# Kernel tuning notes

Hardware: AMD Instinct MI355X
Metric: run time of the kernel (lower is better)

Reference implementation:

```python
import jax, jax.numpy as jnp
import numpy as np

S, D, H, E, A = 30, 200, 200, 1024, 6
B, T = 1024, 64


def setup_inputs() -> dict:
    key = jax.random.key(0)
    ks = jax.random.split(key, 32)
    rn = lambda k, sh, sc=0.05: jax.random.normal(k, sh, dtype=jnp.float32) * sc
    inp = {
        'embed': rn(ks[0], (B, T, E), 1.0),
        'action': rn(ks[1], (B, T, A), 1.0),
        'noise_prior': rn(ks[2], (T, B, S), 1.0),
        'noise_post': rn(ks[3], (T, B, S), 1.0),
        # img1: Dense(hidden) on [stoch+action]
        'w_img1': rn(ks[4], (S + A, H)), 'b_img1': jnp.zeros((H,), jnp.float32),
        # GRUCell(deter): kernel [in,3*D] (z,r,h order), recurrent kernel, 2 biases (reset_after=True)
        'gru_w': rn(ks[5], (H, 3 * D)), 'gru_u': rn(ks[6], (D, 3 * D)),
        'gru_b': jnp.zeros((3 * D,), jnp.float32), 'gru_rb': jnp.zeros((3 * D,), jnp.float32),
        'w_img2': rn(ks[7], (D, H)), 'b_img2': jnp.zeros((H,), jnp.float32),
        'w_imean': rn(ks[8], (H, S)), 'b_imean': jnp.zeros((S,), jnp.float32),
        'w_istd': rn(ks[9], (H, S)), 'b_istd': jnp.zeros((S,), jnp.float32),
        # obs1: Dense(hidden) on [deter+embed]
        'w_obs1': rn(ks[10], (D + E, H)), 'b_obs1': jnp.zeros((H,), jnp.float32),
        'w_omean': rn(ks[11], (H, S)), 'b_omean': jnp.zeros((S,), jnp.float32),
        'w_ostd': rn(ks[12], (H, S)), 'b_ostd': jnp.zeros((S,), jnp.float32),
    }
    return inp


def _observe(embed, action, noise_prior, noise_post,
             w_img1, b_img1, gru_w, gru_u, gru_b, gru_rb,
             w_img2, b_img2, w_imean, b_imean, w_istd, b_istd,
             w_obs1, b_obs1, w_omean, b_omean, w_ostd, b_ostd):
    elu = jax.nn.elu
    Bsz = action.shape[0]

    def step(carry, xs):
        stoch, deter = carry  # [B,S], [B,D]
        a, e, nz_p, nz_o = xs
        # ---- img_step (prior) ----
        x = elu(jnp.concatenate([stoch, a], -1) @ w_img1 + b_img1)  # [B,H]
        xg = x @ gru_w + gru_b          # [B,3D]
        hg = deter @ gru_u + gru_rb     # [B,3D] (reset_after)
        xz, xr, xh = jnp.split(xg, 3, -1)
        hz, hr, hh = jnp.split(hg, 3, -1)
        z = jax.nn.sigmoid(xz + hz)
        r = jax.nn.sigmoid(xr + hr)
        hhat = jnp.tanh(xh + r * hh)
        deter_n = z * deter + (1.0 - z) * hhat  # [B,D]
        x2 = elu(deter_n @ w_img2 + b_img2)
        pmean = x2 @ w_imean + b_imean
        pstd = jax.nn.softplus(x2 @ w_istd + b_istd) + 0.1
        pstoch = pmean + pstd * nz_p
        # ---- obs_step (posterior) ----
        xo = elu(jnp.concatenate([deter_n, e], -1) @ w_obs1 + b_obs1)
        omean = xo @ w_omean + b_omean
        ostd = jax.nn.softplus(xo @ w_ostd + b_ostd)
        ostoch = omean + ostd * nz_o
        out = jnp.concatenate([omean, ostd, ostoch, deter_n,
                               pmean, pstd, pstoch, deter_n], -1)  # [B, 580]
        return (ostoch, deter_n), out

    init = (jnp.zeros((Bsz, S), embed.dtype), jnp.zeros((Bsz, D), embed.dtype))
    xs = (jnp.transpose(action, (1, 0, 2)), jnp.transpose(embed, (1, 0, 2)),
          noise_prior, noise_post)
    _, ys = jax.lax.scan(step, init, xs)  # [T,B,580]
    return jnp.transpose(ys, (1, 0, 2))   # [B,T,580] = post(mean,std,stoch,deter) ++ prior(...)


def reference(embed, action, noise_prior, noise_post,
              w_img1, b_img1, gru_w, gru_u, gru_b, gru_rb,
              w_img2, b_img2, w_imean, b_imean, w_istd, b_istd,
              w_obs1, b_obs1, w_omean, b_omean, w_ostd, b_ostd):
    return _observe(embed, action, noise_prior, noise_post,
                    w_img1, b_img1, gru_w, gru_u, gru_b, gru_rb,
                    w_img2, b_img2, w_imean, b_imean, w_istd, b_istd,
                    w_obs1, b_obs1, w_omean, b_omean, w_ostd, b_ostd)
```

## Files before the change

### kernel.cpp

```cpp
#include <hip/hip_runtime.h>
#include <cstddef>


typedef __bf16 bf16x8 __attribute__((ext_vector_type(8)));
typedef float  f32x4  __attribute__((ext_vector_type(4)));

#define OFF_K1WT 0
#define OFF_W1F  212992
#define OFF_GWF  226304
#define OFF_GUF  362496
#define OFF_WCF  498688
#define OFF_WHF  591872
#define WS_BF_TOTAL 620544
#define WS_XPRE_BYTES 1241088

__device__ __forceinline__ float elu1(float v){ return v > 0.f ? v : expm1f(v); }
__device__ __forceinline__ float sigm(float v){ return 1.f / (1.f + expf(-v)); }
__device__ __forceinline__ float spls(float v){ return fmaxf(v,0.f) + log1pf(expf(-fabsf(v))); }

__global__ __launch_bounds__(256) void k0_convert(
    const float* __restrict__ w_img1, const float* __restrict__ gru_w,
    const float* __restrict__ gru_u,  const float* __restrict__ w_img2,
    const float* __restrict__ w_imean, const float* __restrict__ w_istd,
    const float* __restrict__ w_obs1, const float* __restrict__ w_omean,
    const float* __restrict__ w_ostd, __bf16* __restrict__ o)
{
  int i = blockIdx.x * 256 + threadIdx.x;
  if (i >= WS_BF_TOTAL) return;
  float v = 0.f;
  if (i < OFF_W1F) {
    int n = i >> 10, k = i & 1023;
    v = (n < 200) ? w_obs1[(size_t)(200 + k) * 200 + n] : 0.f;
  } else if (i < OFF_GWF) {
    int q = i - OFF_W1F;
    int e = q & 7, lane = (q >> 3) & 63, f = q >> 9;
    int kc = f & 1, tt = f >> 1;
    int n  = tt * 16 + (lane & 15);
    int kk = kc * 32 + (lane >> 4) * 8 + e;
    if (n < 200 && kk < 36) v = w_img1[kk * 200 + n];
  } else if (i < OFF_GUF) {
    int q = i - OFF_GWF;
    int e = q & 7, lane = (q >> 3) & 63, f = q >> 9;
    int k = f % 7, tt = f / 7;
    int j  = tt * 16 + (lane & 15);
    int kk = k * 32 + (lane >> 4) * 8 + e;
    if (j < 600 && kk < 200) v = gru_w[kk * 600 + j];
  } else if (i < OFF_WCF) {
    int q = i - OFF_GUF;
    int e = q & 7, lane = (q >> 3) & 63, f = q >> 9;
    int k = f % 7, tt = f / 7;
    int j  = tt * 16 + (lane & 15);
    int kk = k * 32 + (lane >> 4) * 8 + e;
    if (j < 600 && kk < 200) v = gru_u[kk * 600 + j];
  } else if (i < OFF_WHF) {
    int q = i - OFF_WCF;
    int e = q & 7, lane = (q >> 3) & 63, f = q >> 9;
    int k = f % 7, tt = f / 7;
    int kk = k * 32 + (lane >> 4) * 8 + e;
    if (kk < 200) {
      if (tt < 13) {
        int n = tt * 16 + (lane & 15);
        if (n < 200) v = w_img2[kk * 200 + n];
      } else {
        int n = (tt - 13) * 16 + (lane & 15);
        if (n < 200) v = w_obs1[kk * 200 + n];
      }
    }
  } else {
    int q = i - OFF_WHF;
    int e = q & 7, lane = (q >> 3) & 63, f = q >> 9;
    int k = f % 7, tt = f / 7;
    int kk = k * 32 + (lane >> 4) * 8 + e;
    int n = tt * 16 + (lane & 15);
    int h = n >> 5, c = n & 31;
    if (kk < 200 && c < 30) {
      const float* wh = (h == 0) ? w_omean : (h == 1) ? w_ostd : (h == 2) ? w_imean : w_istd;
      v = wh[kk * 30 + c];
    }
  }
  o[i] = (__bf16)v;
}

__global__ __launch_bounds__(256) void k1_embed_gemm(
    const float* __restrict__ embed, const __bf16* __restrict__ wT,
    const float* __restrict__ b_obs1, float* __restrict__ xpre)
{
  __shared__ __align__(16) __bf16 As[64][72];
  __shared__ __align__(16) __bf16 Bs[208][72];
  int tid = threadIdx.x;
  int b = blockIdx.x;
  int wave = tid >> 6, lane = tid & 63;
  int lm = lane & 15, quad = lane >> 4;

  f32x4 acc[13];
#pragma unroll
  for (int n = 0; n < 13; ++n) acc[n] = (f32x4){0.f, 0.f, 0.f, 0.f};

  const float* arow_base = embed + (size_t)b * 64 * 1024;

  for (int ko = 0; ko < 1024; ko += 64) {
#pragma unroll
    for (int p = 0; p < 4; ++p) {
      int v = p * 256 + tid; int row = v >> 4; int c4 = v & 15;
      float4 f = *(const float4*)(arow_base + (size_t)row * 1024 + ko + c4 * 4);
      __bf16* dst = &As[row][c4 * 4];
      dst[0] = (__bf16)f.x; dst[1] = (__bf16)f.y;
      dst[2] = (__bf16)f.z; dst[3] = (__bf16)f.w;
    }
#pragma unroll
    for (int p = 0; p < 13; ++p) {
      int v = p * 256 + tid; int n = v >> 4; int c4 = v & 15;
      ushort4 u = *(const ushort4*)(wT + (size_t)n * 1024 + ko + c4 * 4);
      *(ushort4*)&Bs[n][c4 * 4] = u;
    }
    __syncthreads();
#pragma unroll
    for (int kc = 0; kc < 2; ++kc) {
      bf16x8 a = *(const bf16x8*)&As[16 * wave + lm][kc * 32 + quad * 8];
#pragma unroll
      for (int n = 0; n < 13; ++n) {
        bf16x8 bb = *(const bf16x8*)&Bs[16 * n + lm][kc * 32 + quad * 8];
        acc[n] = __builtin_amdgcn_mfma_f32_16x16x32_bf16(a, bb, acc[n], 0, 0, 0);
      }
    }
    __syncthreads();
  }
  int trow_base = 16 * wave + quad * 4;
#pragma unroll
  for (int n = 0; n < 13; ++n) {
    int col = n * 16 + lm;
    if (col < 200) {
      float bias = b_obs1[col];
#pragma unroll
      for (int r = 0; r < 4; ++r) {
        int trow = trow_base + r;
        xpre[(size_t)trow * (1024 * 200) + (size_t)b * 200 + col] = acc[n][r] + bias;
      }
    }
  }
}

__global__ __launch_bounds__(512) void k2_recurrent(
    const float* __restrict__ action, const float* __restrict__ noise_prior,
    const float* __restrict__ noise_post,
    const float* __restrict__ b_img1, const float* __restrict__ gru_b,
    const float* __restrict__ gru_rb, const float* __restrict__ b_img2,
    const float* __restrict__ b_imean, const float* __restrict__ b_istd,
    const float* __restrict__ b_omean, const float* __restrict__ b_ostd,
    const __bf16* __restrict__ w1F, const __bf16* __restrict__ gwF,
    const __bf16* __restrict__ guF, const __bf16* __restrict__ wcF,
    const __bf16* __restrict__ whF,
    const float* __restrict__ xpre, float* __restrict__ out)
{
  __shared__ __align__(16) __bf16 actin[16][72];
  __shared__ __align__(16) __bf16 xbuf[16][232];
  __shared__ __align__(16) __bf16 dbuf[16][232];
  __shared__ __align__(16) char   ovl[39168];
  __shared__ float biasL[1760];

  const int tid  = threadIdx.x;
  const int wv   = tid >> 6;
  const int lane = tid & 63;
  const int lm   = lane & 15, quad = lane >> 4;
  const int b0   = blockIdx.x * 16;

  __bf16* gg    = (__bf16*)ovl;
  __bf16* x2b   = (__bf16*)ovl;
  __bf16* xob   = (__bf16*)(ovl + 7424);
  float*  headb = (float*)(ovl + 14848);

  for (int i = tid; i < 16 * 72; i += 512) {
    int m = i / 72, c = i - m * 72;
    if (c < 30 || c >= 36) actin[m][c] = (__bf16)0.f;
  }
  for (int i = tid; i < 16 * 232; i += 512) { ((__bf16*)xbuf)[i] = (__bf16)0.f; ((__bf16*)dbuf)[i] = (__bf16)0.f; }
  for (int i = tid; i < 1760; i += 512) {
    float v = 0.f;
    if (i < 208)       { if (i < 200) v = b_img1[i]; }
    else if (i < 816)  { int j = i - 208;  if (j < 600) v = gru_b[j]; }
    else if (i < 1424) { int j = i - 816;  if (j < 600) v = gru_rb[j]; }
    else if (i < 1632) { int j = i - 1424; if (j < 200) v = b_img2[j]; }
    else { int n = i - 1632; int h = n >> 5, c = n & 31;
           if (c < 30) v = ((h == 0) ? b_omean : (h == 1) ? b_ostd : (h == 2) ? b_imean : b_istd)[c]; }
    biasL[i] = v;
  }
  if (tid < 96) {
    int m = tid / 6, k = tid - m * 6;
    actin[m][30 + k] = (__bf16)action[(size_t)(b0 + m) * 384 + k];
  }
  __syncthreads();

  for (int t = 0; t < 64; ++t) {
    for (int tt = wv; tt < 13; tt += 8) {
      const __bf16* bw = w1F + tt * 1024 + lane * 8;
      bf16x8 a0 = *(const bf16x8*)&actin[lm][quad * 8];
      bf16x8 a1 = *(const bf16x8*)&actin[lm][32 + quad * 8];
      bf16x8 bv0 = *(const bf16x8*)(bw);
      bf16x8 bv1 = *(const bf16x8*)(bw + 512);
      f32x4 c = (f32x4){0.f, 0.f, 0.f, 0.f};
      c = __builtin_amdgcn_mfma_f32_16x16x32_bf16(a0, bv0, c, 0, 0, 0);
      c = __builtin_amdgcn_mfma_f32_16x16x32_bf16(a1, bv1, c, 0, 0, 0);
      int col = tt * 16 + lm;
      float bias = biasL[col];
      if (col < 200) {
#pragma unroll
        for (int r = 0; r < 4; ++r) xbuf[quad * 4 + r][col] = (__bf16)elu1(c[r] + bias);
      }
    }
    __syncthreads();

    {
      const int gsel = wv >> 2, wsub = wv & 3;
      const __bf16* WF    = gsel ? guF : gwF;
      const __bf16* Abase = gsel ? &dbuf[0][0] : &xbuf[0][0];
      const int cbase = gsel ? 608 : 0;
      const int bbase = gsel ? 816 : 208;
      bf16x8 af[7];
#pragma unroll
      for (int k = 0; k < 7; ++k) af[k] = *(const bf16x8*)(Abase + lm * 232 + k * 32 + quad * 8);
      for (int tt = wsub; tt < 38; tt += 4) {
        const __bf16* bw = WF + tt * 3584 + lane * 8;
        f32x4 c = (f32x4){0.f, 0.f, 0.f, 0.f};
#pragma unroll
        for (int k = 0; k < 7; ++k) {
          bf16x8 bv = *(const bf16x8*)(bw + k * 512);
          c = __builtin_amdgcn_mfma_f32_16x16x32_bf16(af[k], bv, c, 0, 0, 0);
        }
        int col = tt * 16 + lm;
        float bias = biasL[bbase + col];
#pragma unroll
        for (int r = 0; r < 4; ++r) gg[(quad * 4 + r) * 1224 + cbase + col] = (__bf16)(c[r] + bias);
      }
    }
    __syncthreads();

    for (int idx = tid; idx < 3200; idx += 512) {
      int m = idx / 200, d = idx - m * 200;
      const __bf16* row = gg + m * 1224;
      float xz = (float)row[d],        xr_ = (float)row[200 + d], xh = (float)row[400 + d];
      float hz = (float)row[608 + d],  hr_ = (float)row[808 + d], hh = (float)row[1008 + d];
      float z  = sigm(xz + hz);
      float rr = sigm(xr_ + hr_);
      float hc = tanhf(xh + rr * hh);
      float dn = z * (float)dbuf[m][d] + (1.f - z) * hc;
      dbuf[m][d] = (__bf16)dn;
      size_t ob = ((size_t)(b0 + m) * 64 + t) * 580;
      out[ob + 90 + d]  = dn;
      out[ob + 380 + d] = dn;
    }
    __syncthreads();

    {
      bf16x8 df[7];
#pragma unroll
      for (int k = 0; k < 7; ++k) df[k] = *(const bf16x8*)(&dbuf[lm][0] + k * 32 + quad * 8);
      for (int tt = wv; tt < 26; tt += 8) {
        const __bf16* bw = wcF + tt * 3584 + lane * 8;
        f32x4 c = (f32x4){0.f, 0.f, 0.f, 0.f};
#pragma unroll
        for (int k = 0; k < 7; ++k) {
          bf16x8 bv = *(const bf16x8*)(bw + k * 512);
          c = __builtin_amdgcn_mfma_f32_16x16x32_bf16(df[k], bv, c, 0, 0, 0);
        }
        if (tt < 13) {
          int col = tt * 16 + lm;
          float bias = biasL[1424 + col];
          if (col < 200) {
#pragma unroll
            for (int r = 0; r < 4; ++r) x2b[(quad * 4 + r) * 232 + col] = (__bf16)elu1(c[r] + bias);
          }
        } else {
          int col = (tt - 13) * 16 + lm;
          if (col < 200) {
#pragma unroll
            for (int r = 0; r < 4; ++r) {
              int m2 = quad * 4 + r;
              float pre = c[r] + xpre[((size_t)t * 1024 + b0 + m2) * 200 + col];
              xob[m2 * 232 + col] = (__bf16)elu1(pre);
            }
          }
        }
      }
    }
    __syncthreads();

    {
      const __bf16* Ab = (wv < 4) ? xob : x2b;
      bf16x8 hf[7];
#pragma unroll
      for (int k = 0; k < 7; ++k) hf[k] = *(const bf16x8*)(Ab + lm * 232 + k * 32 + quad * 8);
      const __bf16* bw = whF + wv * 3584 + lane * 8;
      f32x4 c = (f32x4){0.f, 0.f, 0.f, 0.f};
#pragma unroll
      for (int k = 0; k < 7; ++k) {
        bf16x8 bv = *(const bf16x8*)(bw + k * 512);
        c = __builtin_amdgcn_mfma_f32_16x16x32_bf16(hf[k], bv, c, 0, 0, 0);
      }
      int n = wv * 16 + lm;
      float bias = biasL[1632 + n];
#pragma unroll
      for (int r = 0; r < 4; ++r) headb[(quad * 4 + r) * 132 + n] = c[r] + bias;
    }
    __syncthreads();

    if (tid < 480) {
      int m = tid / 30, c = tid - m * 30;
      const float* hb = headb + m * 132;
      float om = hb[c], osr = hb[32 + c], pm = hb[64 + c], psr = hb[96 + c];
      float os = spls(osr);
      float ps = spls(psr) + 0.1f;
      float nzo = noise_post [(size_t)t * 30720 + (b0 + m) * 30 + c];
      float nzp = noise_prior[(size_t)t * 30720 + (b0 + m) * 30 + c];
      float ost = om + os * nzo;
      float pst = pm + ps * nzp;
      actin[m][c] = (__bf16)ost;
      size_t ob = ((size_t)(b0 + m) * 64 + t) * 580;
      out[ob + c]       = om;
      out[ob + 30 + c]  = os;
      out[ob + 60 + c]  = ost;
      out[ob + 290 + c] = pm;
      out[ob + 320 + c] = ps;
      out[ob + 350 + c] = pst;
    } else if (t < 63) {
      for (int j = tid - 480; j < 96; j += 32) {
        int m = j / 6, k = j - m * 6;
        actin[m][30 + k] = (__bf16)action[(size_t)(b0 + m) * 384 + (t + 1) * 6 + k];
      }
    }
    __syncthreads();
  }
}

extern "C" void kernel_launch(void* const* d_in, const int* in_sizes, int n_in,
                              void* d_out, int out_size, void* d_ws, size_t ws_size,
                              hipStream_t stream) {
  const float* embed   = (const float*)d_in[0];
  const float* action  = (const float*)d_in[1];
  const float* nzp     = (const float*)d_in[2];
  const float* nzo     = (const float*)d_in[3];
  const float* w_img1  = (const float*)d_in[4];
  const float* b_img1  = (const float*)d_in[5];
  const float* gru_w   = (const float*)d_in[6];
  const float* gru_u   = (const float*)d_in[7];
  const float* gru_b   = (const float*)d_in[8];
  const float* gru_rb  = (const float*)d_in[9];
  const float* w_img2  = (const float*)d_in[10];
  const float* b_img2  = (const float*)d_in[11];
  const float* w_imean = (const float*)d_in[12];
  const float* b_imean = (const float*)d_in[13];
  const float* w_istd  = (const float*)d_in[14];
  const float* b_istd  = (const float*)d_in[15];
  const float* w_obs1  = (const float*)d_in[16];
  const float* b_obs1  = (const float*)d_in[17];
  const float* w_omean = (const float*)d_in[18];
  const float* b_omean = (const float*)d_in[19];
  const float* w_ostd  = (const float*)d_in[20];
  const float* b_ostd  = (const float*)d_in[21];
  float* out = (float*)d_out;

  __bf16* wbf = (__bf16*)d_ws;
  float* xpre = (float*)((char*)d_ws + WS_XPRE_BYTES);

  k0_convert<<<(WS_BF_TOTAL + 255) / 256, 256, 0, stream>>>(
      w_img1, gru_w, gru_u, w_img2, w_imean, w_istd, w_obs1, w_omean, w_ostd, wbf);

  k1_embed_gemm<<<1024, 256, 0, stream>>>(embed, wbf + OFF_K1WT, b_obs1, xpre);

  k2_recurrent<<<64, 512, 0, stream>>>(
      action, nzp, nzo,
      b_img1, gru_b, gru_rb, b_img2, b_imean, b_istd, b_omean, b_ostd,
      wbf + OFF_W1F, wbf + OFF_GWF, wbf + OFF_GUF, wbf + OFF_WCF, wbf + OFF_WHF,
      xpre, out);
}
```

Before: 1.675 ms.

## Double recurrent block to 1024 threads and prefetch weights, noise and xpre

Raises the recurrent kernel block size from 512 to 1024 threads so each per-step GEMM phase is split across 16 waves instead of 8. Idle waves in the first phase stage the noise tiles into shared memory and preload the obs1 precomputed activations before they are needed. The GRU GEMM loop double-buffers weight fragments from global memory. The MFMA chains are split into two accumulators for more instruction-level parallelism, and tanh is replaced with a sigmoid-based formula. The larger block raises register pressure (at most 64 VGPRs per thread at 1024 threads), which may cause spills given the prefetch buffers.

```diff
diff --git a/kernel.cpp b/kernel.cpp
--- a/kernel.cpp
+++ b/kernel.cpp
@@ -140,7 +140,7 @@
   }
 }
 
-__global__ __launch_bounds__(512) void k2_recurrent(
+__global__ __launch_bounds__(1024) void k2_recurrent(
     const float* __restrict__ action, const float* __restrict__ noise_prior,
     const float* __restrict__ noise_post,
     const float* __restrict__ b_img1, const float* __restrict__ gru_b,
@@ -157,6 +157,7 @@
   __shared__ __align__(16) __bf16 dbuf[16][232];
   __shared__ __align__(16) char   ovl[39168];
   __shared__ float biasL[1760];
+  __shared__ float noiseb[960];
 
   const int tid  = threadIdx.x;
   const int wv   = tid >> 6;
@@ -169,12 +170,12 @@
   __bf16* xob   = (__bf16*)(ovl + 7424);
   float*  headb = (float*)(ovl + 14848);
 
-  for (int i = tid; i < 16 * 72; i += 512) {
+  for (int i = tid; i < 16 * 72; i += 1024) {
     int m = i / 72, c = i - m * 72;
     if (c < 30 || c >= 36) actin[m][c] = (__bf16)0.f;
   }
-  for (int i = tid; i < 16 * 232; i += 512) { ((__bf16*)xbuf)[i] = (__bf16)0.f; ((__bf16*)dbuf)[i] = (__bf16)0.f; }
-  for (int i = tid; i < 1760; i += 512) {
+  for (int i = tid; i < 16 * 232; i += 1024) { ((__bf16*)xbuf)[i] = (__bf16)0.f; ((__bf16*)dbuf)[i] = (__bf16)0.f; }
+  for (int i = tid; i < 1760; i += 1024) {
     float v = 0.f;
     if (i < 208)       { if (i < 200) v = b_img1[i]; }
     else if (i < 816)  { int j = i - 208;  if (j < 600) v = gru_b[j]; }
@@ -191,8 +192,8 @@
   __syncthreads();
 
   for (int t = 0; t < 64; ++t) {
-    for (int tt = wv; tt < 13; tt += 8) {
-      const __bf16* bw = w1F + tt * 1024 + lane * 8;
+    if (wv < 13) {
+      const __bf16* bw = w1F + wv * 1024 + lane * 8;
       bf16x8 a0 = *(const bf16x8*)&actin[lm][quad * 8];
       bf16x8 a1 = *(const bf16x8*)&actin[lm][32 + quad * 8];
       bf16x8 bv0 = *(const bf16x8*)(bw);
@@ -200,17 +201,38 @@
       f32x4 c = (f32x4){0.f, 0.f, 0.f, 0.f};
       c = __builtin_amdgcn_mfma_f32_16x16x32_bf16(a0, bv0, c, 0, 0, 0);
       c = __builtin_amdgcn_mfma_f32_16x16x32_bf16(a1, bv1, c, 0, 0, 0);
-      int col = tt * 16 + lm;
+      int col = wv * 16 + lm;
       float bias = biasL[col];
       if (col < 200) {
 #pragma unroll
         for (int r = 0; r < 4; ++r) xbuf[quad * 4 + r][col] = (__bf16)elu1(c[r] + bias);
       }
-    }
-    __syncthreads();
-
+    } else {
+      int j = (wv - 13) * 64 + lane;
+      const float* np = noise_post  + (size_t)t * 30720 + (size_t)b0 * 30;
+      const float* nq = noise_prior + (size_t)t * 30720 + (size_t)b0 * 30;
+      for (int q = j; q < 480; q += 192) {
+        noiseb[q]       = np[q];
+        noiseb[480 + q] = nq[q];
+      }
+    }
+    __syncthreads();
+
+    float xp[4] = {0.f, 0.f, 0.f, 0.f};
     {
-      const int gsel = wv >> 2, wsub = wv & 3;
+      int tt_xo = (wv >= 13) ? wv : (wv < 10 ? wv + 16 : -1);
+      if (tt_xo >= 0) {
+        int col0 = (tt_xo - 13) * 16 + lm;
+        if (col0 < 200) {
+#pragma unroll
+          for (int r = 0; r < 4; ++r)
+            xp[r] = xpre[((size_t)t * 1024 + b0 + quad * 4 + r) * 200 + col0];
+        }
+      }
+    }
+
+    {
+      const int gsel = wv >> 3, wsub = wv & 7;
       const __bf16* WF    = gsel ? guF : gwF;
       const __bf16* Abase = gsel ? &dbuf[0][0] : &xbuf[0][0];
       const int cbase = gsel ? 608 : 0;
@@ -218,30 +240,47 @@
       bf16x8 af[7];
 #pragma unroll
       for (int k = 0; k < 7; ++k) af[k] = *(const bf16x8*)(Abase + lm * 232 + k * 32 + quad * 8);
-      for (int tt = wsub; tt < 38; tt += 4) {
-        const __bf16* bw = WF + tt * 3584 + lane * 8;
-        f32x4 c = (f32x4){0.f, 0.f, 0.f, 0.f};
-#pragma unroll
-        for (int k = 0; k < 7; ++k) {
-          bf16x8 bv = *(const bf16x8*)(bw + k * 512);
-          c = __builtin_amdgcn_mfma_f32_16x16x32_bf16(af[k], bv, c, 0, 0, 0);
+      bf16x8 cur[7], nxt[7];
+      {
+        const __bf16* bw = WF + (size_t)wsub * 3584 + lane * 8;
+#pragma unroll
+        for (int k = 0; k < 7; ++k) cur[k] = *(const bf16x8*)(bw + k * 512);
+      }
+      for (int tt = wsub; tt < 38; tt += 8) {
+        int tn = tt + 8;
+        if (tn < 38) {
+          const __bf16* bn = WF + (size_t)tn * 3584 + lane * 8;
+#pragma unroll
+          for (int k = 0; k < 7; ++k) nxt[k] = *(const bf16x8*)(bn + k * 512);
         }
+        f32x4 c0 = (f32x4){0.f, 0.f, 0.f, 0.f};
+        f32x4 c1 = (f32x4){0.f, 0.f, 0.f, 0.f};
+        c0 = __builtin_amdgcn_mfma_f32_16x16x32_bf16(af[0], cur[0], c0, 0, 0, 0);
+        c1 = __builtin_amdgcn_mfma_f32_16x16x32_bf16(af[1], cur[1], c1, 0, 0, 0);
+        c0 = __builtin_amdgcn_mfma_f32_16x16x32_bf16(af[2], cur[2], c0, 0, 0, 0);
+        c1 = __builtin_amdgcn_mfma_f32_16x16x32_bf16(af[3], cur[3], c1, 0, 0, 0);
+        c0 = __builtin_amdgcn_mfma_f32_16x16x32_bf16(af[4], cur[4], c0, 0, 0, 0);
+        c1 = __builtin_amdgcn_mfma_f32_16x16x32_bf16(af[5], cur[5], c1, 0, 0, 0);
+        c0 = __builtin_amdgcn_mfma_f32_16x16x32_bf16(af[6], cur[6], c0, 0, 0, 0);
+        f32x4 c = c0 + c1;
         int col = tt * 16 + lm;
         float bias = biasL[bbase + col];
 #pragma unroll
         for (int r = 0; r < 4; ++r) gg[(quad * 4 + r) * 1224 + cbase + col] = (__bf16)(c[r] + bias);
-      }
-    }
-    __syncthreads();
-
-    for (int idx = tid; idx < 3200; idx += 512) {
+#pragma unroll
+        for (int k = 0; k < 7; ++k) cur[k] = nxt[k];
+      }
+    }
+    __syncthreads();
+
+    for (int idx = tid; idx < 3200; idx += 1024) {
       int m = idx / 200, d = idx - m * 200;
       const __bf16* row = gg + m * 1224;
       float xz = (float)row[d],        xr_ = (float)row[200 + d], xh = (float)row[400 + d];
       float hz = (float)row[608 + d],  hr_ = (float)row[808 + d], hh = (float)row[1008 + d];
       float z  = sigm(xz + hz);
       float rr = sigm(xr_ + hr_);
-      float hc = tanhf(xh + rr * hh);
+      float hc = 2.f * sigm(2.f * (xh + rr * hh)) - 1.f;
       float dn = z * (float)dbuf[m][d] + (1.f - z) * hc;
       dbuf[m][d] = (__bf16)dn;
       size_t ob = ((size_t)(b0 + m) * 64 + t) * 580;
@@ -254,14 +293,21 @@
       bf16x8 df[7];
 #pragma unroll
       for (int k = 0; k < 7; ++k) df[k] = *(const bf16x8*)(&dbuf[lm][0] + k * 32 + quad * 8);
-      for (int tt = wv; tt < 26; tt += 8) {
-        const __bf16* bw = wcF + tt * 3584 + lane * 8;
-        f32x4 c = (f32x4){0.f, 0.f, 0.f, 0.f};
-#pragma unroll
-        for (int k = 0; k < 7; ++k) {
-          bf16x8 bv = *(const bf16x8*)(bw + k * 512);
-          c = __builtin_amdgcn_mfma_f32_16x16x32_bf16(df[k], bv, c, 0, 0, 0);
-        }
+      for (int tt = wv; tt < 26; tt += 16) {
+        const __bf16* bw = wcF + (size_t)tt * 3584 + lane * 8;
+        bf16x8 bv[7];
+#pragma unroll
+        for (int k = 0; k < 7; ++k) bv[k] = *(const bf16x8*)(bw + k * 512);
+        f32x4 c0 = (f32x4){0.f, 0.f, 0.f, 0.f};
+        f32x4 c1 = (f32x4){0.f, 0.f, 0.f, 0.f};
+        c0 = __builtin_amdgcn_mfma_f32_16x16x32_bf16(df[0], bv[0], c0, 0, 0, 0);
+        c1 = __builtin_amdgcn_mfma_f32_16x16x32_bf16(df[1], bv[1], c1, 0, 0, 0);
+        c0 = __builtin_amdgcn_mfma_f32_16x16x32_bf16(df[2], bv[2], c0, 0, 0, 0);
+        c1 = __builtin_amdgcn_mfma_f32_16x16x32_bf16(df[3], bv[3], c1, 0, 0, 0);
+        c0 = __builtin_amdgcn_mfma_f32_16x16x32_bf16(df[4], bv[4], c0, 0, 0, 0);
+        c1 = __builtin_amdgcn_mfma_f32_16x16x32_bf16(df[5], bv[5], c1, 0, 0, 0);
+        c0 = __builtin_amdgcn_mfma_f32_16x16x32_bf16(df[6], bv[6], c0, 0, 0, 0);
+        f32x4 c = c0 + c1;
         if (tt < 13) {
           int col = tt * 16 + lm;
           float bias = biasL[1424 + col];
@@ -275,8 +321,7 @@
 #pragma unroll
             for (int r = 0; r < 4; ++r) {
               int m2 = quad * 4 + r;
-              float pre = c[r] + xpre[((size_t)t * 1024 + b0 + m2) * 200 + col];
-              xob[m2 * 232 + col] = (__bf16)elu1(pre);
+              xob[m2 * 232 + col] = (__bf16)elu1(c[r] + xp[r]);
             }
           }
         }
@@ -284,18 +329,25 @@
     }
     __syncthreads();
 
-    {
+    if (wv < 8) {
       const __bf16* Ab = (wv < 4) ? xob : x2b;
       bf16x8 hf[7];
 #pragma unroll
       for (int k = 0; k < 7; ++k) hf[k] = *(const bf16x8*)(Ab + lm * 232 + k * 32 + quad * 8);
       const __bf16* bw = whF + wv * 3584 + lane * 8;
-      f32x4 c = (f32x4){0.f, 0.f, 0.f, 0.f};
-#pragma unroll
-      for (int k = 0; k < 7; ++k) {
-        bf16x8 bv = *(const bf16x8*)(bw + k * 512);
-        c = __builtin_amdgcn_mfma_f32_16x16x32_bf16(hf[k], bv, c, 0, 0, 0);
-      }
+      bf16x8 bv[7];
+#pragma unroll
+      for (int k = 0; k < 7; ++k) bv[k] = *(const bf16x8*)(bw + k * 512);
+      f32x4 c0 = (f32x4){0.f, 0.f, 0.f, 0.f};
+      f32x4 c1 = (f32x4){0.f, 0.f, 0.f, 0.f};
+      c0 = __builtin_amdgcn_mfma_f32_16x16x32_bf16(hf[0], bv[0], c0, 0, 0, 0);
+      c1 = __builtin_amdgcn_mfma_f32_16x16x32_bf16(hf[1], bv[1], c1, 0, 0, 0);
+      c0 = __builtin_amdgcn_mfma_f32_16x16x32_bf16(hf[2], bv[2], c0, 0, 0, 0);
+      c1 = __builtin_amdgcn_mfma_f32_16x16x32_bf16(hf[3], bv[3], c1, 0, 0, 0);
+      c0 = __builtin_amdgcn_mfma_f32_16x16x32_bf16(hf[4], bv[4], c0, 0, 0, 0);
+      c1 = __builtin_amdgcn_mfma_f32_16x16x32_bf16(hf[5], bv[5], c1, 0, 0, 0);
+      c0 = __builtin_amdgcn_mfma_f32_16x16x32_bf16(hf[6], bv[6], c0, 0, 0, 0);
+      f32x4 c = c0 + c1;
       int n = wv * 16 + lm;
       float bias = biasL[1632 + n];
 #pragma unroll
@@ -309,8 +361,8 @@
       float om = hb[c], osr = hb[32 + c], pm = hb[64 + c], psr = hb[96 + c];
       float os = spls(osr);
       float ps = spls(psr) + 0.1f;
-      float nzo = noise_post [(size_t)t * 30720 + (b0 + m) * 30 + c];
-      float nzp = noise_prior[(size_t)t * 30720 + (b0 + m) * 30 + c];
+      float nzo = noiseb[tid];
+      float nzp = noiseb[480 + tid];
       float ost = om + os * nzo;
       float pst = pm + ps * nzp;
       actin[m][c] = (__bf16)ost;
@@ -321,11 +373,10 @@
       out[ob + 290 + c] = pm;
       out[ob + 320 + c] = ps;
       out[ob + 350 + c] = pst;
-    } else if (t < 63) {
-      for (int j = tid - 480; j < 96; j += 32) {
-        int m = j / 6, k = j - m * 6;
-        actin[m][30 + k] = (__bf16)action[(size_t)(b0 + m) * 384 + (t + 1) * 6 + k];
-      }
+    } else if (tid < 576 && t < 63) {
+      int j = tid - 480;
+      int m = j / 6, k = j - m * 6;
+      actin[m][30 + k] = (__bf16)action[(size_t)(b0 + m) * 384 + (t + 1) * 6 + k];
     }
     __syncthreads();
   }
@@ -366,7 +417,7 @@
 
   k1_embed_gemm<<<1024, 256, 0, stream>>>(embed, wbf + OFF_K1WT, b_obs1, xpre);
 
-  k2_recurrent<<<64, 512, 0, stream>>>(
+  k2_recurrent<<<64, 1024, 0, stream>>>(
       action, nzp, nzo,
       b_img1, gru_b, gru_rb, b_img2, b_imean, b_istd, b_omean, b_ostd,
       wbf + OFF_W1F, wbf + OFF_GWF, wbf + OFF_GUF, wbf + OFF_WCF, wbf + OFF_WHF,
```

After: 1.517 ms. -9.4%, faster.
